# Performance work log

Hardware: AMD Instinct MI355X
Metric: run time of the kernel (lower is better)

## Reference

```python
import jax, jax.numpy as jnp
import numpy as np

N, K, F, W = 32768, 32, 4, 256

def setup_inputs() -> dict:
    key = jax.random.key(0)
    ks = jax.random.split(key, 12)
    init = lambda k, shape, fan_in: jax.random.normal(k, shape, jnp.float32) / np.sqrt(fan_in)
    return {
        "h_center": jax.random.normal(ks[0], (N, W), jnp.float32),
        "h_neighbors": jax.random.normal(ks[1], (N, K, W), jnp.float32),
        "differences": jax.random.normal(ks[2], (N, K, F), jnp.float32),
        # filter MLP (depth=2): Dense(W) -> silu -> Dense(W)
        "W_f1": init(ks[3], (F, W), F),
        "b_f1": jnp.zeros((W,), jnp.float32),
        "W_f2": init(ks[4], (W, W), W),
        "b_f2": jnp.zeros((W,), jnp.float32),
        # neighbor projection Dense(W)
        "W_nb": init(ks[5], (W, W), W),
        "b_nb": jnp.zeros((W,), jnp.float32),
        # center projection Dense(W)
        "W_c": init(ks[6], (W, W), W),
        "b_c": jnp.zeros((W,), jnp.float32),
    }

def reference(h_center, h_neighbors, differences, W_f1, b_f1, W_f2, b_f2, W_nb, b_nb, W_c, b_c):
    # filter MLP over edge (difference) features: [N,K,F] -> [N,K,W]
    f = jax.nn.silu(differences @ W_f1 + b_f1)
    filter_kernel = f @ W_f2 + b_f2
    # project neighbor features: [N,K,W]
    h_nb = h_neighbors @ W_nb + b_nb
    # gated message, sum over neighbor axis -> [N,W]
    msg = jnp.sum(filter_kernel * h_nb, axis=-2)
    # center dense + message, silu
    h_out = jax.nn.silu(h_center @ W_c + b_c + msg)
    return h_out
```

## Files before the change

### kernel.cpp

```cpp
#include <hip/hip_runtime.h>
#include <hip/hip_bf16.h>
#include <stdint.h>

#define NN 32768
#define KNBR 32

typedef __attribute__((ext_vector_type(8))) short short8;
typedef __attribute__((ext_vector_type(4))) float f32x4;

__device__ __forceinline__ unsigned int f2bf(float x) {
    union { float f; unsigned int u; } c; c.f = x;
    return (c.u + 0x7FFFu + ((c.u >> 16) & 1u)) >> 16;
}
__device__ __forceinline__ unsigned int pk2(float a, float b) {
    return f2bf(a) | (f2bf(b) << 16);
}
__device__ __forceinline__ unsigned int pkr(float a, float b) {
    unsigned ua = __float_as_uint(a) + 0x8000u;
    unsigned ub = __float_as_uint(b) + 0x8000u;
    return (ua >> 16) | (ub & 0xFFFF0000u);
}
__device__ __forceinline__ float silu_f(float x) {
    return x / (1.0f + __expf(-x));
}

__global__ void prep_weights(const float* __restrict__ Wf2,
                             const float* __restrict__ Wnb,
                             const float* __restrict__ Wc,
                             uint4* __restrict__ ws_out) {
    int t = blockIdx.x * 256 + threadIdx.x;
    int w = t >> 13;
    int q = t & 8191;
    int kt = q >> 10;
    int nt = (q >> 6) & 15;
    int lane = q & 63;
    int k0 = kt * 32 + ((lane >> 4) << 3);
    int col = nt * 16 + (lane & 15);
    const float* src = (w == 0) ? Wf2 : (w == 1) ? Wnb : Wc;
    const float* p = src + (size_t)k0 * 256 + col;
    uint4 o;
    o.x = pk2(p[0],        p[256]);
    o.y = pk2(p[512],      p[768]);
    o.z = pk2(p[1024],     p[1280]);
    o.w = pk2(p[1536],     p[1792]);
    ws_out[t] = o;
}

__global__ __launch_bounds__(256) void prep_f(
        const float* __restrict__ diff,
        const float* __restrict__ Wf1,
        const float* __restrict__ b1,
        uint4* __restrict__ fout)
{
    const int bid  = blockIdx.x;
    const int kt   = bid & 7;
    const size_t g128 = (size_t)(bid >> 3);
    const int tid  = threadIdx.x;
    const int lane = tid & 63;
    const int wv   = tid >> 6;
    const int kgrp = lane >> 4, r16 = lane & 15;
    const int k0   = kt * 32 + kgrp * 8;

    float4 cwa[4], cwb[4];
    #pragma unroll
    for (int j = 0; j < 4; ++j) {
        cwa[j] = *(const float4*)(Wf1 + j * 256 + k0);
        cwb[j] = *(const float4*)(Wf1 + j * 256 + k0 + 4);
    }
    const float4 cba = *(const float4*)(b1 + k0);
    const float4 cbb = *(const float4*)(b1 + k0 + 4);

    #pragma unroll
    for (int mi = 0; mi < 2; ++mi) {
        const int mt = mi * 4 + wv;
        const size_t row = g128 * 128 + mt * 16 + r16;
        const float4 d = *(const float4*)(diff + row * 4);
        float v0 = cba.x + d.x*cwa[0].x + d.y*cwa[1].x + d.z*cwa[2].x + d.w*cwa[3].x;
        float v1 = cba.y + d.x*cwa[0].y + d.y*cwa[1].y + d.z*cwa[2].y + d.w*cwa[3].y;
        float v2 = cba.z + d.x*cwa[0].z + d.y*cwa[1].z + d.z*cwa[2].z + d.w*cwa[3].z;
        float v3 = cba.w + d.x*cwa[0].w + d.y*cwa[1].w + d.z*cwa[2].w + d.w*cwa[3].w;
        float v4 = cbb.x + d.x*cwb[0].x + d.y*cwb[1].x + d.z*cwb[2].x + d.w*cwb[3].x;
        float v5 = cbb.y + d.x*cwb[0].y + d.y*cwb[1].y + d.z*cwb[2].y + d.w*cwb[3].y;
        float v6 = cbb.z + d.x*cwb[0].z + d.y*cwb[1].z + d.z*cwb[2].z + d.w*cwb[3].z;
        float v7 = cbb.w + d.x*cwb[0].w + d.y*cwb[1].w + d.z*cwb[2].w + d.w*cwb[3].w;
        uint4 o;
        o.x = pkr(silu_f(v0), silu_f(v1));
        o.y = pkr(silu_f(v2), silu_f(v3));
        o.z = pkr(silu_f(v4), silu_f(v5));
        o.w = pkr(silu_f(v6), silu_f(v7));
        fout[(size_t)bid * 512 + mt * 64 + lane] = o;
    }
}

__global__ __launch_bounds__(1024, 4) void msg_kernel(
        const float* __restrict__ nbr,
        const float* __restrict__ b2,
        const float* __restrict__ bnb,
        const uint4* __restrict__ wf2_g,
        const uint4* __restrict__ wnb_g,
        const uint4* __restrict__ ffrag,
        float* __restrict__ msg_out)
{
    __shared__ uint4 w2l[4096];
    __shared__ uint4 wnl[4096];
    __shared__ uint4 ebuf[2][512];

    const int tid  = threadIdx.x;
    const int lane = tid & 63;
    const int wid  = tid >> 6;
    const int wm   = wid >> 2;
    const int wn   = wid & 3;
    const int xcd  = blockIdx.x & 7;
    const int yy   = blockIdx.x >> 3;
    const int chalf = yy & 1;
    const int rgrp  = xcd * 32 + (yy >> 1);
    const size_t rowbase = (size_t)rgrp * 4096;
    const int colbase = chalf * 128;

    const int s    = tid >> 1;
    const int half = tid & 1;
    const int emt  = s >> 6;
    const int ekg  = (s >> 4) & 3;
    const int erow = s & 15;

    auto eload = [&](int g) -> float4 {
        const int t = g >> 3, kt = g & 7;
        return *(const float4*)(nbr + (rowbase + (size_t)t * 128 + emt * 16 + erow) * 256
                                + kt * 32 + ekg * 8 + half * 4);
    };
    auto ewrite = [&](int pb, const float4& v) {
        unsigned lo = pkr(v.x, v.y), hi = pkr(v.z, v.w);
        *(unsigned long long*)((char*)&ebuf[pb][s] + half * 8) =
            ((unsigned long long)hi << 32) | lo;
    };
    const short8* fbase = (const short8*)ffrag;
    auto fload = [&](int g, short8& a0, short8& a1) {
        const size_t fb = ((size_t)(rgrp * 32 + (g >> 3)) * 8 + (g & 7)) * 512;
        a0 = fbase[fb + (wm * 2 + 0) * 64 + lane];
        a1 = fbase[fb + (wm * 2 + 1) * 64 + lane];
    };

    #pragma unroll
    for (int i = 0; i < 4; ++i) {
        int idx = tid + i * 1024;
        int kt = idx >> 9, rem = idx & 511;
        int src = kt * 1024 + chalf * 512 + rem;
        w2l[idx] = wf2_g[src];
        wnl[idx] = wnb_g[src];
    }
    float vb2[2], vbn[2];
    #pragma unroll
    for (int n = 0; n < 2; ++n) {
        const int col = colbase + wn * 32 + n * 16 + (lane & 15);
        vb2[n] = b2[col];
        vbn[n] = bnb[col];
    }
    ewrite(0, eload(0));
    float4 EnA = eload(1);
    short8 aF0c, aF1c;
    fload(0, aF0c, aF1c);
    __syncthreads();

    f32x4 accP[2][2], accH[2][2];
    #pragma unroll
    for (int m = 0; m < 2; ++m)
        #pragma unroll
        for (int n = 0; n < 2; ++n) {
            accP[m][n] = (f32x4){0.f, 0.f, 0.f, 0.f};
            accH[m][n] = (f32x4){0.f, 0.f, 0.f, 0.f};
        }

    const short8* w28 = (const short8*)w2l;
    const short8* wn8 = (const short8*)wnl;

    for (int t = 0; t < 32; ++t) {
        #pragma unroll
        for (int kt = 0; kt < 8; ++kt) {
            const int g = t * 8 + kt;
            const int pb = g & 1;
            float4 EfA;
            if (g + 2 < 256) EfA = eload(g + 2);
            short8 aF0n, aF1n;
            if (g + 1 < 256) fload(g + 1, aF0n, aF1n);
            const short8* eb8 = (const short8*)ebuf[pb];
            short8 aE0 = eb8[(wm * 2 + 0) * 64 + lane];
            short8 aE1 = eb8[(wm * 2 + 1) * 64 + lane];
            short8 B20 = w28[(kt * 8 + wn * 2 + 0) * 64 + lane];
            short8 B21 = w28[(kt * 8 + wn * 2 + 1) * 64 + lane];
            short8 Bn0 = wn8[(kt * 8 + wn * 2 + 0) * 64 + lane];
            short8 Bn1 = wn8[(kt * 8 + wn * 2 + 1) * 64 + lane];
            accP[0][0] = __builtin_amdgcn_mfma_f32_16x16x32_bf16(aF0c, B20, accP[0][0], 0, 0, 0);
            accP[0][1] = __builtin_amdgcn_mfma_f32_16x16x32_bf16(aF0c, B21, accP[0][1], 0, 0, 0);
            accP[1][0] = __builtin_amdgcn_mfma_f32_16x16x32_bf16(aF1c, B20, accP[1][0], 0, 0, 0);
            accP[1][1] = __builtin_amdgcn_mfma_f32_16x16x32_bf16(aF1c, B21, accP[1][1], 0, 0, 0);
            accH[0][0] = __builtin_amdgcn_mfma_f32_16x16x32_bf16(aE0, Bn0, accH[0][0], 0, 0, 0);
            accH[0][1] = __builtin_amdgcn_mfma_f32_16x16x32_bf16(aE0, Bn1, accH[0][1], 0, 0, 0);
            accH[1][0] = __builtin_amdgcn_mfma_f32_16x16x32_bf16(aE1, Bn0, accH[1][0], 0, 0, 0);
            accH[1][1] = __builtin_amdgcn_mfma_f32_16x16x32_bf16(aE1, Bn1, accH[1][1], 0, 0, 0);
            if (g + 1 < 256) ewrite(pb ^ 1, EnA);
            if (kt == 7) {
                const size_t node = (size_t)rgrp * 128 + t * 4 + wm;
                #pragma unroll
                for (int n = 0; n < 2; ++n) {
                    float sv = 0.f;
                    #pragma unroll
                    for (int m = 0; m < 2; ++m)
                        #pragma unroll
                        for (int r = 0; r < 4; ++r)
                            sv += (accP[m][n][r] + vb2[n]) * (accH[m][n][r] + vbn[n]);
                    sv += __shfl_xor(sv, 16);
                    sv += __shfl_xor(sv, 32);
                    if (lane < 16)
                        msg_out[node * 256 + colbase + wn * 32 + n * 16 + lane] = sv;
                }
                #pragma unroll
                for (int m = 0; m < 2; ++m)
                    #pragma unroll
                    for (int n = 0; n < 2; ++n) {
                        accP[m][n] = (f32x4){0.f, 0.f, 0.f, 0.f};
                        accH[m][n] = (f32x4){0.f, 0.f, 0.f, 0.f};
                    }
            }
            asm volatile("s_waitcnt lgkmcnt(0)" ::: "memory");
            __builtin_amdgcn_sched_barrier(0);
            __builtin_amdgcn_s_barrier();
            EnA = EfA;
            aF0c = aF0n; aF1c = aF1n;
        }
    }
}

__global__ __launch_bounds__(256) void out_kernel(
        const float* __restrict__ hc,
        const float* __restrict__ bc,
        const uint4* __restrict__ wc_g,
        float* __restrict__ out)
{
    __shared__ unsigned short a_s[4 * 2 * 64 * 8];
    __shared__ unsigned short wc_s[2 * 16 * 64 * 8];

    const int tid  = threadIdx.x;
    const int lane = tid & 63;
    const int wn   = tid >> 6;
    const int rblk = blockIdx.x * 64;

    f32x4 acc[4][4];
    #pragma unroll
    for (int mt = 0; mt < 4; ++mt)
        #pragma unroll
        for (int nt = 0; nt < 4; ++nt)
            acc[mt][nt] = (f32x4){0.f, 0.f, 0.f, 0.f};

    uint4* af4 = (uint4*)a_s;
    for (int kt2 = 0; kt2 < 4; ++kt2) {
        {
            int row = tid >> 2, quarter = tid & 3;
            const float* src = hc + (size_t)(rblk + row) * 256 + kt2 * 64 + quarter * 16;
            float4 v0 = *(const float4*)(src + 0);
            float4 v1 = *(const float4*)(src + 4);
            float4 v2 = *(const float4*)(src + 8);
            float4 v3 = *(const float4*)(src + 12);
            uint4 p0, p1;
            p0.x = pk2(v0.x, v0.y); p0.y = pk2(v0.z, v0.w);
            p0.z = pk2(v1.x, v1.y); p0.w = pk2(v1.z, v1.w);
            p1.x = pk2(v2.x, v2.y); p1.y = pk2(v2.z, v2.w);
            p1.z = pk2(v3.x, v3.y); p1.w = pk2(v3.z, v3.w);
            int mt = row >> 4, kti = quarter >> 1, fr = row & 15;
            int g0 = (quarter & 1) * 2;
            af4[(mt * 2 + kti) * 64 + g0 * 16 + fr]       = p0;
            af4[(mt * 2 + kti) * 64 + (g0 + 1) * 16 + fr] = p1;
            const uint4* srcw = wc_g + kt2 * 2048;
            uint4* dw = (uint4*)wc_s;
            #pragma unroll
            for (int j = 0; j < 8; ++j)
                dw[j * 256 + tid] = srcw[j * 256 + tid];
        }
        __syncthreads();
        #pragma unroll
        for (int kti = 0; kti < 2; ++kti) {
            short8 b[4];
            #pragma unroll
            for (int nt = 0; nt < 4; ++nt)
                b[nt] = *(const short8*)&wc_s[((kti * 16 + wn * 4 + nt) * 64 + lane) * 8];
            #pragma unroll
            for (int mt = 0; mt < 4; ++mt) {
                short8 a = *(const short8*)&a_s[((mt * 2 + kti) * 64 + lane) * 8];
                #pragma unroll
                for (int nt = 0; nt < 4; ++nt)
                    acc[mt][nt] = __builtin_amdgcn_mfma_f32_16x16x32_bf16(a, b[nt], acc[mt][nt], 0, 0, 0);
            }
        }
        __syncthreads();
    }

    #pragma unroll
    for (int mt = 0; mt < 4; ++mt)
        #pragma unroll
        for (int nt = 0; nt < 4; ++nt)
            #pragma unroll
            for (int r = 0; r < 4; ++r) {
                int grow = rblk + mt * 16 + ((lane >> 4) << 2) + r;
                int col  = wn * 64 + nt * 16 + (lane & 15);
                size_t idx = (size_t)grow * 256 + col;
                float v = acc[mt][nt][r] + bc[col] + out[idx];
                out[idx] = silu_f(v);
            }
}

extern "C" void kernel_launch(void* const* d_in, const int* in_sizes, int n_in,
                              void* d_out, int out_size, void* d_ws, size_t ws_size,
                              hipStream_t stream) {
    const float* h_center    = (const float*)d_in[0];
    const float* h_neighbors = (const float*)d_in[1];
    const float* differences = (const float*)d_in[2];
    const float* W_f1        = (const float*)d_in[3];
    const float* b_f1        = (const float*)d_in[4];
    const float* W_f2        = (const float*)d_in[5];
    const float* b_f2        = (const float*)d_in[6];
    const float* W_nb        = (const float*)d_in[7];
    const float* b_nb        = (const float*)d_in[8];
    const float* W_c         = (const float*)d_in[9];
    const float* b_c         = (const float*)d_in[10];
    float* out = (float*)d_out;

    uint4* ws4 = (uint4*)d_ws;
    const uint4* wf2_ws = ws4;
    const uint4* wnb_ws = ws4 + 8192;
    const uint4* wc_ws  = ws4 + 16384;
    uint4* f_ws         = ws4 + 24576;

    prep_weights<<<96, 256, 0, stream>>>(W_f2, W_nb, W_c, ws4);
    prep_f<<<65536, 256, 0, stream>>>(differences, W_f1, b_f1, f_ws);
    msg_kernel<<<512, 1024, 0, stream>>>(
        h_neighbors, b_f2, b_nb, wf2_ws, wnb_ws, f_ws, out);
    out_kernel<<<NN / 64, 256, 0, stream>>>(h_center, b_c, wc_ws, out);
}
```

Before: 709.9 us.

## Load neighbor A-fragments directly into registers, drop LDS staging and per-step barrier

Each wave now loads its own neighbor-feature MFMA A fragments straight from global memory into registers and converts them to bf16 in place. This replaces the cooperative load into a double-buffered LDS tile. It removes the LDS writes and reads and the block-wide barrier on every k-step, so waves run independently. In exchange, each wave does more, narrower global loads, with 32-byte chunks per lane spread across rows, and holds more registers for prefetch. Cross-wave sharing of the loaded tile is lost, since waves with the same wm but different wn load the same data redundantly.

```diff
diff --git a/kernel.cpp b/kernel.cpp
--- a/kernel.cpp
+++ b/kernel.cpp
@@ -19,6 +19,12 @@
     unsigned ua = __float_as_uint(a) + 0x8000u;
     unsigned ub = __float_as_uint(b) + 0x8000u;
     return (ua >> 16) | (ub & 0xFFFF0000u);
+}
+__device__ __forceinline__ short8 cvt8(const float4& a, const float4& b) {
+    union { unsigned u[4]; short8 s; } r;
+    r.u[0] = pkr(a.x, a.y); r.u[1] = pkr(a.z, a.w);
+    r.u[2] = pkr(b.x, b.y); r.u[3] = pkr(b.z, b.w);
+    return r.s;
 }
 __device__ __forceinline__ float silu_f(float x) {
     return x / (1.0f + __expf(-x));
@@ -103,7 +109,6 @@
 {
     __shared__ uint4 w2l[4096];
     __shared__ uint4 wnl[4096];
-    __shared__ uint4 ebuf[2][512];
 
     const int tid  = threadIdx.x;
     const int lane = tid & 63;
@@ -117,29 +122,6 @@
     const size_t rowbase = (size_t)rgrp * 4096;
     const int colbase = chalf * 128;
 
-    const int s    = tid >> 1;
-    const int half = tid & 1;
-    const int emt  = s >> 6;
-    const int ekg  = (s >> 4) & 3;
-    const int erow = s & 15;
-
-    auto eload = [&](int g) -> float4 {
-        const int t = g >> 3, kt = g & 7;
-        return *(const float4*)(nbr + (rowbase + (size_t)t * 128 + emt * 16 + erow) * 256
-                                + kt * 32 + ekg * 8 + half * 4);
-    };
-    auto ewrite = [&](int pb, const float4& v) {
-        unsigned lo = pkr(v.x, v.y), hi = pkr(v.z, v.w);
-        *(unsigned long long*)((char*)&ebuf[pb][s] + half * 8) =
-            ((unsigned long long)hi << 32) | lo;
-    };
-    const short8* fbase = (const short8*)ffrag;
-    auto fload = [&](int g, short8& a0, short8& a1) {
-        const size_t fb = ((size_t)(rgrp * 32 + (g >> 3)) * 8 + (g & 7)) * 512;
-        a0 = fbase[fb + (wm * 2 + 0) * 64 + lane];
-        a1 = fbase[fb + (wm * 2 + 1) * 64 + lane];
-    };
-
     #pragma unroll
     for (int i = 0; i < 4; ++i) {
         int idx = tid + i * 1024;
@@ -155,11 +137,24 @@
         vb2[n] = b2[col];
         vbn[n] = bnb[col];
     }
-    ewrite(0, eload(0));
-    float4 EnA = eload(1);
-    short8 aF0c, aF1c;
-    fload(0, aF0c, aF1c);
     __syncthreads();
+
+    const float* ebase = nbr + (rowbase + wm * 32 + (lane & 15)) * 256
+                         + ((lane >> 4) << 3);
+    const short8* fbase = (const short8*)ffrag;
+
+    auto eload4 = [&](int g, float4* v) {
+        const float* p = ebase + (size_t)(g >> 3) * 32768 + (g & 7) * 32;
+        v[0] = *(const float4*)p;
+        v[1] = *(const float4*)(p + 4);
+        v[2] = *(const float4*)(p + 4096);
+        v[3] = *(const float4*)(p + 4100);
+    };
+    auto fload = [&](int g, short8& a0, short8& a1) {
+        const size_t fb = (size_t)(rgrp * 256 + g) * 512;
+        a0 = fbase[fb + (wm * 2 + 0) * 64 + lane];
+        a1 = fbase[fb + (wm * 2 + 1) * 64 + lane];
+    };
 
     f32x4 accP[2][2], accH[2][2];
     #pragma unroll
@@ -173,18 +168,21 @@
     const short8* w28 = (const short8*)w2l;
     const short8* wn8 = (const short8*)wnl;
 
+    short8 aF0c, aF1c, aF0n, aF1n;
+    float4 Ec[4], En[4];
+    fload(0, aF0c, aF1c);
+    eload4(0, Ec);
+
     for (int t = 0; t < 32; ++t) {
         #pragma unroll
         for (int kt = 0; kt < 8; ++kt) {
             const int g = t * 8 + kt;
-            const int pb = g & 1;
-            float4 EfA;
-            if (g + 2 < 256) EfA = eload(g + 2);
-            short8 aF0n, aF1n;
-            if (g + 1 < 256) fload(g + 1, aF0n, aF1n);
-            const short8* eb8 = (const short8*)ebuf[pb];
-            short8 aE0 = eb8[(wm * 2 + 0) * 64 + lane];
-            short8 aE1 = eb8[(wm * 2 + 1) * 64 + lane];
+            if (g + 1 < 256) {
+                fload(g + 1, aF0n, aF1n);
+                eload4(g + 1, En);
+            }
+            short8 aE0 = cvt8(Ec[0], Ec[1]);
+            short8 aE1 = cvt8(Ec[2], Ec[3]);
             short8 B20 = w28[(kt * 8 + wn * 2 + 0) * 64 + lane];
             short8 B21 = w28[(kt * 8 + wn * 2 + 1) * 64 + lane];
             short8 Bn0 = wn8[(kt * 8 + wn * 2 + 0) * 64 + lane];
@@ -197,7 +195,6 @@
             accH[0][1] = __builtin_amdgcn_mfma_f32_16x16x32_bf16(aE0, Bn1, accH[0][1], 0, 0, 0);
             accH[1][0] = __builtin_amdgcn_mfma_f32_16x16x32_bf16(aE1, Bn0, accH[1][0], 0, 0, 0);
             accH[1][1] = __builtin_amdgcn_mfma_f32_16x16x32_bf16(aE1, Bn1, accH[1][1], 0, 0, 0);
-            if (g + 1 < 256) ewrite(pb ^ 1, EnA);
             if (kt == 7) {
                 const size_t node = (size_t)rgrp * 128 + t * 4 + wm;
                 #pragma unroll
@@ -221,11 +218,8 @@
                         accH[m][n] = (f32x4){0.f, 0.f, 0.f, 0.f};
                     }
             }
-            asm volatile("s_waitcnt lgkmcnt(0)" ::: "memory");
-            __builtin_amdgcn_sched_barrier(0);
-            __builtin_amdgcn_s_barrier();
-            EnA = EfA;
             aF0c = aF0n; aF1c = aF1n;
+            Ec[0] = En[0]; Ec[1] = En[1]; Ec[2] = En[2]; Ec[3] = En[3];
         }
     }
 }
```

New measurement: 2.075 ms. 192% more time.

## Retile msg_kernel into 512-thread blocks over column quarters with 4x1 wave tiles

Applied to the files above, without the earlier changes.

Splits the message kernel into twice as many half-sized blocks, each covering 64 output columns instead of 128. Each wave now computes four row tiles against one column tile, and each thread loads a full 8-element neighbor chunk. LDS weight storage per block is halved and more blocks can be resident. In exchange, each neighbor row and filter fragment is fetched by four blocks instead of two, increasing global/L2 traffic.

```diff
diff --git a/kernel.cpp b/kernel.cpp
--- a/kernel.cpp
+++ b/kernel.cpp
@@ -92,7 +92,7 @@
     }
 }
 
-__global__ __launch_bounds__(1024, 4) void msg_kernel(
+__global__ __launch_bounds__(512, 4) void msg_kernel(
         const float* __restrict__ nbr,
         const float* __restrict__ b2,
         const float* __restrict__ bnb,
@@ -101,8 +101,8 @@
         const uint4* __restrict__ ffrag,
         float* __restrict__ msg_out)
 {
-    __shared__ uint4 w2l[4096];
-    __shared__ uint4 wnl[4096];
+    __shared__ uint4 w2l[2048];
+    __shared__ uint4 wnl[2048];
     __shared__ uint4 ebuf[2][512];
 
     const int tid  = threadIdx.x;
@@ -111,64 +111,60 @@
     const int wm   = wid >> 2;
     const int wn   = wid & 3;
     const int xcd  = blockIdx.x & 7;
-    const int yy   = blockIdx.x >> 3;
-    const int chalf = yy & 1;
-    const int rgrp  = xcd * 32 + (yy >> 1);
+    const int ii   = blockIdx.x >> 3;
+    const int rgrp = xcd * 32 + (ii >> 2);
+    const int colq = ii & 3;
     const size_t rowbase = (size_t)rgrp * 4096;
-    const int colbase = chalf * 128;
-
-    const int s    = tid >> 1;
-    const int half = tid & 1;
-    const int emt  = s >> 6;
-    const int ekg  = (s >> 4) & 3;
-    const int erow = s & 15;
-
-    auto eload = [&](int g) -> float4 {
-        const int t = g >> 3, kt = g & 7;
-        return *(const float4*)(nbr + (rowbase + (size_t)t * 128 + emt * 16 + erow) * 256
-                                + kt * 32 + ekg * 8 + half * 4);
+    const int colbase = colq * 64;
+
+    #pragma unroll
+    for (int j = 0; j < 4; ++j) {
+        int idx = tid + j * 512;
+        int kt = idx >> 8, ln = (idx >> 6) & 3, la = idx & 63;
+        int src = (kt * 16 + colq * 4 + ln) * 64 + la;
+        w2l[idx] = wf2_g[src];
+        wnl[idx] = wnb_g[src];
+    }
+    const float vb2 = b2[colbase + wn * 16 + (lane & 15)];
+    const float vbn = bnb[colbase + wn * 16 + (lane & 15)];
+
+    const int srow = (tid >> 6) * 16 + (lane & 15);
+    const int skoct = (lane >> 4);
+    auto eload = [&](int g, float4& a, float4& b) {
+        const float* p = nbr + (rowbase + (size_t)(g >> 3) * 128 + srow) * 256
+                         + (g & 7) * 32 + skoct * 8;
+        a = *(const float4*)p;
+        b = *(const float4*)(p + 4);
     };
-    auto ewrite = [&](int pb, const float4& v) {
-        unsigned lo = pkr(v.x, v.y), hi = pkr(v.z, v.w);
-        *(unsigned long long*)((char*)&ebuf[pb][s] + half * 8) =
-            ((unsigned long long)hi << 32) | lo;
+    auto ewrite = [&](int pb, const float4& a, const float4& b) {
+        uint4 o;
+        o.x = pkr(a.x, a.y); o.y = pkr(a.z, a.w);
+        o.z = pkr(b.x, b.y); o.w = pkr(b.z, b.w);
+        ebuf[pb][tid] = o;
     };
     const short8* fbase = (const short8*)ffrag;
-    auto fload = [&](int g, short8& a0, short8& a1) {
-        const size_t fb = ((size_t)(rgrp * 32 + (g >> 3)) * 8 + (g & 7)) * 512;
-        a0 = fbase[fb + (wm * 2 + 0) * 64 + lane];
-        a1 = fbase[fb + (wm * 2 + 1) * 64 + lane];
+    auto fload = [&](int g, short8* a) {
+        const size_t fb = (size_t)(rgrp * 256 + g) * 512;
+        #pragma unroll
+        for (int m = 0; m < 4; ++m)
+            a[m] = fbase[fb + (wm * 4 + m) * 64 + lane];
     };
 
-    #pragma unroll
-    for (int i = 0; i < 4; ++i) {
-        int idx = tid + i * 1024;
-        int kt = idx >> 9, rem = idx & 511;
-        int src = kt * 1024 + chalf * 512 + rem;
-        w2l[idx] = wf2_g[src];
-        wnl[idx] = wnb_g[src];
-    }
-    float vb2[2], vbn[2];
-    #pragma unroll
-    for (int n = 0; n < 2; ++n) {
-        const int col = colbase + wn * 32 + n * 16 + (lane & 15);
-        vb2[n] = b2[col];
-        vbn[n] = bnb[col];
-    }
-    ewrite(0, eload(0));
-    float4 EnA = eload(1);
-    short8 aF0c, aF1c;
-    fload(0, aF0c, aF1c);
+    float4 e0a, e0b;
+    eload(0, e0a, e0b);
+    ewrite(0, e0a, e0b);
+    short8 aFc[4], aFn[4];
+    fload(0, aFc);
+    float4 EnA, EnB, EfA, EfB;
+    eload(1, EnA, EnB);
     __syncthreads();
 
-    f32x4 accP[2][2], accH[2][2];
-    #pragma unroll
-    for (int m = 0; m < 2; ++m)
-        #pragma unroll
-        for (int n = 0; n < 2; ++n) {
-            accP[m][n] = (f32x4){0.f, 0.f, 0.f, 0.f};
-            accH[m][n] = (f32x4){0.f, 0.f, 0.f, 0.f};
-        }
+    f32x4 accP[4], accH[4];
+    #pragma unroll
+    for (int m = 0; m < 4; ++m) {
+        accP[m] = (f32x4){0.f, 0.f, 0.f, 0.f};
+        accH[m] = (f32x4){0.f, 0.f, 0.f, 0.f};
+    }
 
     const short8* w28 = (const short8*)w2l;
     const short8* wn8 = (const short8*)wnl;
@@ -178,54 +174,52 @@
         for (int kt = 0; kt < 8; ++kt) {
             const int g = t * 8 + kt;
             const int pb = g & 1;
-            float4 EfA;
-            if (g + 2 < 256) EfA = eload(g + 2);
-            short8 aF0n, aF1n;
-            if (g + 1 < 256) fload(g + 1, aF0n, aF1n);
+            if (g + 2 < 256) eload(g + 2, EfA, EfB);
+            if (g + 1 < 256) fload(g + 1, aFn);
             const short8* eb8 = (const short8*)ebuf[pb];
-            short8 aE0 = eb8[(wm * 2 + 0) * 64 + lane];
-            short8 aE1 = eb8[(wm * 2 + 1) * 64 + lane];
-            short8 B20 = w28[(kt * 8 + wn * 2 + 0) * 64 + lane];
-            short8 B21 = w28[(kt * 8 + wn * 2 + 1) * 64 + lane];
-            short8 Bn0 = wn8[(kt * 8 + wn * 2 + 0) * 64 + lane];
-            short8 Bn1 = wn8[(kt * 8 + wn * 2 + 1) * 64 + lane];
-            accP[0][0] = __builtin_amdgcn_mfma_f32_16x16x32_bf16(aF0c, B20, accP[0][0], 0, 0, 0);
-            accP[0][1] = __builtin_amdgcn_mfma_f32_16x16x32_bf16(aF0c, B21, accP[0][1], 0, 0, 0);
-            accP[1][0] = __builtin_amdgcn_mfma_f32_16x16x32_bf16(aF1c, B20, accP[1][0], 0, 0, 0);
-            accP[1][1] = __builtin_amdgcn_mfma_f32_16x16x32_bf16(aF1c, B21, accP[1][1], 0, 0, 0);
-            accH[0][0] = __builtin_amdgcn_mfma_f32_16x16x32_bf16(aE0, Bn0, accH[0][0], 0, 0, 0);
-            accH[0][1] = __builtin_amdgcn_mfma_f32_16x16x32_bf16(aE0, Bn1, accH[0][1], 0, 0, 0);
-            accH[1][0] = __builtin_amdgcn_mfma_f32_16x16x32_bf16(aE1, Bn0, accH[1][0], 0, 0, 0);
-            accH[1][1] = __builtin_amdgcn_mfma_f32_16x16x32_bf16(aE1, Bn1, accH[1][1], 0, 0, 0);
-            if (g + 1 < 256) ewrite(pb ^ 1, EnA);
+            short8 B2 = w28[(kt * 4 + wn) * 64 + lane];
+            short8 Bn = wn8[(kt * 4 + wn) * 64 + lane];
+            short8 aE0 = eb8[(wm * 4 + 0) * 64 + lane];
+            short8 aE1 = eb8[(wm * 4 + 1) * 64 + lane];
+            short8 aE2 = eb8[(wm * 4 + 2) * 64 + lane];
+            short8 aE3 = eb8[(wm * 4 + 3) * 64 + lane];
+            accP[0] = __builtin_amdgcn_mfma_f32_16x16x32_bf16(aFc[0], B2, accP[0], 0, 0, 0);
+            accP[1] = __builtin_amdgcn_mfma_f32_16x16x32_bf16(aFc[1], B2, accP[1], 0, 0, 0);
+            accP[2] = __builtin_amdgcn_mfma_f32_16x16x32_bf16(aFc[2], B2, accP[2], 0, 0, 0);
+            accP[3] = __builtin_amdgcn_mfma_f32_16x16x32_bf16(aFc[3], B2, accP[3], 0, 0, 0);
+            accH[0] = __builtin_amdgcn_mfma_f32_16x16x32_bf16(aE0, Bn, accH[0], 0, 0, 0);
+            accH[1] = __builtin_amdgcn_mfma_f32_16x16x32_bf16(aE1, Bn, accH[1], 0, 0, 0);
+            accH[2] = __builtin_amdgcn_mfma_f32_16x16x32_bf16(aE2, Bn, accH[2], 0, 0, 0);
+            accH[3] = __builtin_amdgcn_mfma_f32_16x16x32_bf16(aE3, Bn, accH[3], 0, 0, 0);
+            if (g + 1 < 256) ewrite(pb ^ 1, EnA, EnB);
             if (kt == 7) {
-                const size_t node = (size_t)rgrp * 128 + t * 4 + wm;
                 #pragma unroll
-                for (int n = 0; n < 2; ++n) {
+                for (int h = 0; h < 2; ++h) {
+                    const size_t node = (size_t)rgrp * 128 + t * 4 + wm * 2 + h;
                     float sv = 0.f;
                     #pragma unroll
-                    for (int m = 0; m < 2; ++m)
+                    for (int m2 = 0; m2 < 2; ++m2) {
+                        const int m = h * 2 + m2;
                         #pragma unroll
                         for (int r = 0; r < 4; ++r)
-                            sv += (accP[m][n][r] + vb2[n]) * (accH[m][n][r] + vbn[n]);
+                            sv += (accP[m][r] + vb2) * (accH[m][r] + vbn);
+                    }
                     sv += __shfl_xor(sv, 16);
                     sv += __shfl_xor(sv, 32);
                     if (lane < 16)
-                        msg_out[node * 256 + colbase + wn * 32 + n * 16 + lane] = sv;
+                        msg_out[node * 256 + colbase + wn * 16 + lane] = sv;
                 }
                 #pragma unroll
-                for (int m = 0; m < 2; ++m)
-                    #pragma unroll
-                    for (int n = 0; n < 2; ++n) {
-                        accP[m][n] = (f32x4){0.f, 0.f, 0.f, 0.f};
-                        accH[m][n] = (f32x4){0.f, 0.f, 0.f, 0.f};
-                    }
+                for (int m = 0; m < 4; ++m) {
+                    accP[m] = (f32x4){0.f, 0.f, 0.f, 0.f};
+                    accH[m] = (f32x4){0.f, 0.f, 0.f, 0.f};
+                }
             }
             asm volatile("s_waitcnt lgkmcnt(0)" ::: "memory");
             __builtin_amdgcn_sched_barrier(0);
             __builtin_amdgcn_s_barrier();
-            EnA = EfA;
-            aF0c = aF0n; aF1c = aF1n;
+            EnA = EfA; EnB = EfB;
+            aFc[0] = aFn[0]; aFc[1] = aFn[1]; aFc[2] = aFn[2]; aFc[3] = aFn[3];
         }
     }
 }
@@ -331,7 +325,7 @@
 
     prep_weights<<<96, 256, 0, stream>>>(W_f2, W_nb, W_c, ws4);
     prep_f<<<65536, 256, 0, stream>>>(differences, W_f1, b_f1, f_ws);
-    msg_kernel<<<512, 1024, 0, stream>>>(
+    msg_kernel<<<1024, 512, 0, stream>>>(
         h_neighbors, b_f2, b_nb, wf2_ws, wnb_ws, f_ws, out);
     out_kernel<<<NN / 64, 256, 0, stream>>>(h_center, b_c, wc_ws, out);
 }
```

New measurement: 993.6 us. +40.0%, slower.
